# Optimization experiments

Hardware: AMD Instinct MI355X
Metric: run time of the kernel (lower is better)

## Reference

```python
import jax, jax.numpy as jnp
import numpy as np

NUM_USERS = 100000
NUM_ITEMS = 50000
N_NODES = NUM_USERS + NUM_ITEMS
EMBED_DIM = 64
NUM_LAYERS = 3
NUM_EDGES = 1250000
EDGE_ATTR_DIM = 7
MLP_HID = 32
AUDIO_SCALE = 1.0
META_SCALE = 0.5


def _l2norm(x, eps=1e-12):
    # F.normalize(p=2, dim=-1): x / max(||x||, eps)
    n = jnp.sqrt(jnp.sum(x * x, axis=-1, keepdims=True))
    return x / jnp.maximum(n, eps)


def setup_inputs() -> dict:
    key = jax.random.key(0)
    ks = jax.random.split(key, 12)
    return {
        'user_emb_w': jax.random.normal(ks[0], (NUM_USERS, EMBED_DIM), jnp.float32),
        'artist_emb_w': jax.random.normal(ks[1], (20000, EMBED_DIM), jnp.float32),
        'album_emb_w': jax.random.normal(ks[2], (40000, EMBED_DIM), jnp.float32),
        'item_audio': jax.random.normal(ks[3], (NUM_ITEMS, EMBED_DIM), jnp.float32),
        'edge_attr': jax.random.normal(ks[4], (NUM_EDGES, EDGE_ATTR_DIM), jnp.float32),
        'edge_weight_init': jax.random.uniform(ks[5], (NUM_EDGES,), jnp.float32),
        'w1': jax.random.normal(ks[6], (EDGE_ATTR_DIM + 1, MLP_HID), jnp.float32),
        'b1': jnp.zeros((MLP_HID,), jnp.float32),
        'w2': jax.random.normal(ks[7], (MLP_HID, 1), jnp.float32),
        'b2': jnp.zeros((1,), jnp.float32),
        'edge_index': jax.random.randint(ks[8], (2, NUM_EDGES), 0, N_NODES, jnp.int64 if jax.config.read('jax_enable_x64') else jnp.int32),
        'artist_ids': jax.random.randint(ks[9], (NUM_ITEMS,), 0, 20000, jnp.int32),
        'album_ids': jax.random.randint(ks[10], (NUM_ITEMS,), 0, 40000, jnp.int32),
    }


def reference(user_emb_w, artist_emb_w, album_emb_w, item_audio, edge_attr,
              edge_weight_init, w1, b1, w2, b2, edge_index, artist_ids, album_ids):
    # Edge weight MLP: Linear -> ReLU -> Linear -> Sigmoid, squeezed
    ef = jnp.concatenate([edge_attr, edge_weight_init[:, None]], axis=1)  # [E, 8]
    h = jax.nn.relu(ef @ w1 + b1)
    w = jax.nn.sigmoid(h @ w2 + b2)[:, 0]  # [E]

    # Node features
    user_embed = _l2norm(user_emb_w)                                   # [U, D]
    meta = (artist_emb_w[artist_ids] + album_emb_w[album_ids]) * META_SCALE
    item_embed = _l2norm(item_audio * AUDIO_SCALE + meta)              # [I, D]
    x = jnp.concatenate([user_embed, item_embed], axis=0)              # [N, D]

    # gcn_norm (LGConv default, no self-loops): deg from target (col) scatter of w
    row, col = edge_index[0], edge_index[1]
    deg = jax.ops.segment_sum(w, col, num_segments=N_NODES)
    dinv = jnp.where(deg > 0, jax.lax.rsqrt(jnp.maximum(deg, 1e-30)), 0.0)
    norm = dinv[row] * w * dinv[col]                                   # [E]

    acc = x
    for _ in range(NUM_LAYERS):
        msg = norm[:, None] * x[row]                                   # [E, D]
        x = jax.ops.segment_sum(msg, col, num_segments=N_NODES)       # [N, D]
        acc = acc + x
    x = _l2norm(acc / (NUM_LAYERS + 1))

    user_emb = x[:NUM_USERS]
    item_emb = x[NUM_USERS:]
    align_loss = jnp.float32(0.0)
    return user_emb, item_emb, align_loss
```

## Files before the change

### kernel.cpp

```cpp
#include <hip/hip_runtime.h>
#include <hip/hip_bf16.h>
#include <math.h>

#define NUM_USERS  100000
#define NUM_ITEMS  50000
#define N_NODES    150000
#define EMBED_DIM  64
#define NUM_EDGES  1250000
#define MLP_HID    32
#define SCAN_B     1024
#define SCAN_NB    ((N_NODES + SCAN_B - 1) / SCAN_B)

__global__ void hist_rank(const int* __restrict__ edge_index,
                          int* __restrict__ cnt,
                          int* __restrict__ rank) {
    int e = blockIdx.x * blockDim.x + threadIdx.x;
    if (e >= NUM_EDGES) return;
    int c = edge_index[NUM_EDGES + e];
    rank[e] = atomicAdd(&cnt[c], 1);
}

__global__ void scan_partial(const int* __restrict__ cnt,
                             int* __restrict__ part) {
    __shared__ int s[SCAN_B];
    int tid = threadIdx.x;
    int i = blockIdx.x * SCAN_B + tid;
    s[tid] = (i < N_NODES) ? cnt[i] : 0;
    __syncthreads();
#pragma unroll
    for (int off = SCAN_B / 2; off > 0; off >>= 1) {
        if (tid < off) s[tid] += s[tid + off];
        __syncthreads();
    }
    if (tid == 0) part[blockIdx.x] = s[0];
}

__global__ void scan_offsets(const int* __restrict__ part,
                             int* __restrict__ base_off) {
    __shared__ int s[256];
    int tid = threadIdx.x;
    int v = (tid < SCAN_NB) ? part[tid] : 0;
    s[tid] = v;
    __syncthreads();
#pragma unroll
    for (int off = 1; off < 256; off <<= 1) {
        int t = (tid >= off) ? s[tid - off] : 0;
        __syncthreads();
        s[tid] += t;
        __syncthreads();
    }
    if (tid < SCAN_NB) base_off[tid] = s[tid] - v;
}

__global__ void scan_apply(const int* __restrict__ cnt,
                           const int* __restrict__ base_off,
                           int* __restrict__ row_ptr) {
    __shared__ int s[SCAN_B];
    int tid = threadIdx.x;
    int i = blockIdx.x * SCAN_B + tid;
    int v = (i < N_NODES) ? cnt[i] : 0;
    s[tid] = v;
    __syncthreads();
    for (int off = 1; off < SCAN_B; off <<= 1) {
        int t = (tid >= off) ? s[tid - off] : 0;
        __syncthreads();
        s[tid] += t;
        __syncthreads();
    }
    if (i < N_NODES) row_ptr[i] = s[tid] - v + base_off[blockIdx.x];
    if (blockIdx.x == 0 && tid == 0) row_ptr[N_NODES] = NUM_EDGES;
}

__global__ void mlp_scatter(const float* __restrict__ edge_attr,
                            const float* __restrict__ ew,
                            const float* __restrict__ w1,
                            const float* __restrict__ b1,
                            const float* __restrict__ w2,
                            const float* __restrict__ b2,
                            const int*   __restrict__ edge_index,
                            const int*   __restrict__ rank,
                            const int*   __restrict__ row_ptr,
                            int2* __restrict__ csr_pair) {
    __shared__ float w1s[8 * MLP_HID];
    __shared__ float b1s[MLP_HID];
    __shared__ float w2s[MLP_HID];
    int tid = threadIdx.x;
    if (tid < 8 * MLP_HID) w1s[tid] = w1[tid];
    if (tid < MLP_HID) { b1s[tid] = b1[tid]; w2s[tid] = w2[tid]; }
    __syncthreads();

    int e = blockIdx.x * blockDim.x + tid;
    if (e >= NUM_EDGES) return;

    float ef[8];
#pragma unroll
    for (int k = 0; k < 7; ++k) ef[k] = edge_attr[e * 7 + k];
    ef[7] = ew[e];

    float s = b2[0];
#pragma unroll
    for (int j = 0; j < MLP_HID; ++j) {
        float h = b1s[j];
#pragma unroll
        for (int k = 0; k < 8; ++k) h = fmaf(ef[k], w1s[k * MLP_HID + j], h);
        h = fmaxf(h, 0.0f);
        s = fmaf(h, w2s[j], s);
    }
    float w = 1.0f / (1.0f + expf(-s));

    int r = edge_index[e];
    int c = edge_index[NUM_EDGES + e];
    int pos = row_ptr[c] + rank[e];
    int2 pr;
    pr.x = r;
    pr.y = __float_as_int(w);
    csr_pair[pos] = pr;
}

__global__ void deg_dinv_csr(const int* __restrict__ row_ptr,
                             const int2* __restrict__ csr_pair,
                             float* __restrict__ dinv) {
    int t = blockIdx.x * blockDim.x + threadIdx.x;
    int node = t >> 4;
    int lane = t & 15;
    if (node >= N_NODES) return;
    int s = row_ptr[node], e = row_ptr[node + 1];
    float sum = 0.0f;
    for (int j = s + lane; j < e; j += 16) sum += __int_as_float(csr_pair[j].y);
    sum += __shfl_xor(sum, 8);
    sum += __shfl_xor(sum, 4);
    sum += __shfl_xor(sum, 2);
    sum += __shfl_xor(sum, 1);
    if (lane == 0)
        dinv[node] = (sum > 0.0f) ? rsqrtf(fmaxf(sum, 1e-30f)) : 0.0f;
}

__global__ void csr_scale(const int* __restrict__ row_ptr,
                          const float* __restrict__ dinv,
                          int2* __restrict__ csr_pair) {
    int t = blockIdx.x * blockDim.x + threadIdx.x;
    int node = t >> 4;
    int lane = t & 15;
    if (node >= N_NODES) return;
    int s = row_ptr[node], e = row_ptr[node + 1];
    float dc = dinv[node];
    for (int j = s + lane; j < e; j += 16) {
        int2 p = csr_pair[j];
        p.y = __float_as_int(__int_as_float(p.y) * dc * dinv[p.x]);
        csr_pair[j] = p;
    }
}

__global__ void init_x(const float* __restrict__ user_w,
                       const float* __restrict__ artist_w,
                       const float* __restrict__ album_w,
                       const float* __restrict__ audio,
                       const int*   __restrict__ artist_ids,
                       const int*   __restrict__ album_ids,
                       __hip_bfloat16* __restrict__ x) {
    int t = blockIdx.x * blockDim.x + threadIdx.x;
    int row = t >> 6;
    int lane = t & 63;
    if (row >= N_NODES) return;

    float v;
    if (row < NUM_USERS) {
        v = user_w[row * EMBED_DIM + lane];
    } else {
        int r = row - NUM_USERS;
        int ar = artist_ids[r];
        int al = album_ids[r];
        v = audio[r * EMBED_DIM + lane]
          + 0.5f * (artist_w[ar * EMBED_DIM + lane] + album_w[al * EMBED_DIM + lane]);
    }
    float ss = v * v;
#pragma unroll
    for (int off = 32; off > 0; off >>= 1) ss += __shfl_xor(ss, off);
    float scale = 1.0f / fmaxf(sqrtf(ss), 1e-12f);
    x[row * EMBED_DIM + lane] = __float2bfloat16(v * scale);
}

__global__ void propagate_mid(const int* __restrict__ row_ptr,
                              const int2* __restrict__ csr_pair,
                              const unsigned short* __restrict__ xin,
                              unsigned short* __restrict__ xout) {
    int t = blockIdx.x * blockDim.x + threadIdx.x;
    int node = t >> 6;
    int lane = t & 63;
    if (node >= N_NODES) return;

    int start = row_ptr[node];
    int end   = row_ptr[node + 1];

    int eg = lane >> 4;
    int dq = (lane & 15) << 2;

    float a0 = 0, a1 = 0, a2 = 0, a3 = 0;

    int j = start + eg;
    int2 p = csr_pair[j];

    for (int base = start; base < end; base += 4) {
        bool ok = (base + eg < end);
        int   src = ok ? p.x : 0;
        float nw  = ok ? __int_as_float(p.y) : 0.0f;
        uint2 u = *(const uint2*)(xin + ((size_t)src << 6) + dq);
        j += 4;
        int2 pn = csr_pair[j];
        a0 = fmaf(nw, __uint_as_float(u.x << 16),         a0);
        a1 = fmaf(nw, __uint_as_float(u.x & 0xffff0000u), a1);
        a2 = fmaf(nw, __uint_as_float(u.y << 16),         a2);
        a3 = fmaf(nw, __uint_as_float(u.y & 0xffff0000u), a3);
        p = pn;
    }

    a0 += __shfl_xor(a0, 16); a1 += __shfl_xor(a1, 16);
    a2 += __shfl_xor(a2, 16); a3 += __shfl_xor(a3, 16);
    a0 += __shfl_xor(a0, 32); a1 += __shfl_xor(a1, 32);
    a2 += __shfl_xor(a2, 32); a3 += __shfl_xor(a3, 32);

    if (eg == 0) {
        size_t o = ((size_t)node << 6) + dq;
        unsigned int b0 = (unsigned int)__bfloat16_as_ushort(__float2bfloat16(a0));
        unsigned int b1 = (unsigned int)__bfloat16_as_ushort(__float2bfloat16(a1));
        unsigned int b2 = (unsigned int)__bfloat16_as_ushort(__float2bfloat16(a2));
        unsigned int b3 = (unsigned int)__bfloat16_as_ushort(__float2bfloat16(a3));
        uint2 u;
        u.x = b0 | (b1 << 16);
        u.y = b2 | (b3 << 16);
        *(uint2*)(xout + o) = u;
    }
}

__global__ void propagate_final(const int* __restrict__ row_ptr,
                                const int2* __restrict__ csr_pair,
                                const unsigned short* __restrict__ x0,
                                const unsigned short* __restrict__ x1,
                                const unsigned short* __restrict__ x2,
                                float* __restrict__ outp) {
    int t = blockIdx.x * blockDim.x + threadIdx.x;
    int node = t >> 6;
    int lane = t & 63;
    if (node >= N_NODES) return;

    int start = row_ptr[node];
    int end   = row_ptr[node + 1];

    int eg = lane >> 4;
    int dq = (lane & 15) << 2;

    float a0 = 0, a1 = 0, a2 = 0, a3 = 0;

    int j = start + eg;
    int2 p = csr_pair[j];

    for (int base = start; base < end; base += 4) {
        bool ok = (base + eg < end);
        int   src = ok ? p.x : 0;
        float nw  = ok ? __int_as_float(p.y) : 0.0f;
        uint2 u = *(const uint2*)(x2 + ((size_t)src << 6) + dq);
        j += 4;
        int2 pn = csr_pair[j];
        a0 = fmaf(nw, __uint_as_float(u.x << 16),         a0);
        a1 = fmaf(nw, __uint_as_float(u.x & 0xffff0000u), a1);
        a2 = fmaf(nw, __uint_as_float(u.y << 16),         a2);
        a3 = fmaf(nw, __uint_as_float(u.y & 0xffff0000u), a3);
        p = pn;
    }

    a0 += __shfl_xor(a0, 16); a1 += __shfl_xor(a1, 16);
    a2 += __shfl_xor(a2, 16); a3 += __shfl_xor(a3, 16);
    a0 += __shfl_xor(a0, 32); a1 += __shfl_xor(a1, 32);
    a2 += __shfl_xor(a2, 32); a3 += __shfl_xor(a3, 32);

    if (eg == 0) {
        size_t o = ((size_t)node << 6) + dq;
        uint2 u0 = *(const uint2*)(x0 + o);
        uint2 u1 = *(const uint2*)(x1 + o);
        uint2 u2 = *(const uint2*)(x2 + o);

#define BF_LO(u) __uint_as_float((u) << 16)
#define BF_HI(u) __uint_as_float((u) & 0xffff0000u)
        float v0 = (BF_LO(u0.x) + BF_LO(u1.x) + BF_LO(u2.x) + a0) * 0.25f;
        float v1 = (BF_HI(u0.x) + BF_HI(u1.x) + BF_HI(u2.x) + a1) * 0.25f;
        float v2 = (BF_LO(u0.y) + BF_LO(u1.y) + BF_LO(u2.y) + a2) * 0.25f;
        float v3 = (BF_HI(u0.y) + BF_HI(u1.y) + BF_HI(u2.y) + a3) * 0.25f;
#undef BF_LO
#undef BF_HI

        float ss = v0 * v0 + v1 * v1 + v2 * v2 + v3 * v3;
        ss += __shfl_xor(ss, 1);
        ss += __shfl_xor(ss, 2);
        ss += __shfl_xor(ss, 4);
        ss += __shfl_xor(ss, 8);
        float scale = 1.0f / fmaxf(sqrtf(ss), 1e-12f);

        float4 r = { v0 * scale, v1 * scale, v2 * scale, v3 * scale };
        *(float4*)(outp + o) = r;
    }
    if (blockIdx.x == 0 && threadIdx.x == 0)
        outp[(size_t)N_NODES * EMBED_DIM] = 0.0f;
}

extern "C" void kernel_launch(void* const* d_in, const int* in_sizes, int n_in,
                              void* d_out, int out_size, void* d_ws, size_t ws_size,
                              hipStream_t stream) {
    const float* user_w     = (const float*)d_in[0];
    const float* artist_w   = (const float*)d_in[1];
    const float* album_w    = (const float*)d_in[2];
    const float* audio      = (const float*)d_in[3];
    const float* edge_attr  = (const float*)d_in[4];
    const float* ew         = (const float*)d_in[5];
    const float* w1         = (const float*)d_in[6];
    const float* b1         = (const float*)d_in[7];
    const float* w2         = (const float*)d_in[8];
    const float* b2         = (const float*)d_in[9];
    const int*   edge_index = (const int*)d_in[10];
    const int*   artist_ids = (const int*)d_in[11];
    const int*   album_ids  = (const int*)d_in[12];
    float* out = (float*)d_out;

    float* ws = (float*)d_ws;
    unsigned short* x0 = (unsigned short*)ws;
    unsigned short* x1 = (unsigned short*)(ws + 4800000);
    unsigned short* x2 = (unsigned short*)(ws + 9600000);
    int*  row_ptr  = (int*)(ws + 14400000);
    int2* csr_pair = (int2*)(ws + 14560000);
    float* dinv    = ws + 17060000;
    int*   cnt     = (int*)ws;
    int*   rank    = (int*)(ws + 150000);
    int*   part    = (int*)(ws + 1400000);
    int*   baseoff = (int*)(ws + 1401000);

    const int B = 256;
    const int egrid = (NUM_EDGES + B - 1) / B;
    const int ngrid   = (N_NODES * EMBED_DIM) / B;
    const int ngrid16 = (N_NODES * 16) / B;

    hipMemsetAsync(cnt, 0, N_NODES * sizeof(int), stream);

    hist_rank<<<egrid, B, 0, stream>>>(edge_index, cnt, rank);

    scan_partial<<<SCAN_NB, SCAN_B, 0, stream>>>(cnt, part);
    scan_offsets<<<1, 256, 0, stream>>>(part, baseoff);
    scan_apply<<<SCAN_NB, SCAN_B, 0, stream>>>(cnt, baseoff, row_ptr);

    mlp_scatter<<<egrid, B, 0, stream>>>(
        edge_attr, ew, w1, b1, w2, b2, edge_index, rank, row_ptr, csr_pair);

    deg_dinv_csr<<<ngrid16, B, 0, stream>>>(row_ptr, csr_pair, dinv);
    csr_scale<<<ngrid16, B, 0, stream>>>(row_ptr, dinv, csr_pair);

    init_x<<<ngrid, B, 0, stream>>>(
        user_w, artist_w, album_w, audio, artist_ids, album_ids,
        (__hip_bfloat16*)x0);

    propagate_mid<<<ngrid, B, 0, stream>>>(row_ptr, csr_pair, x0, x1);
    propagate_mid<<<ngrid, B, 0, stream>>>(row_ptr, csr_pair, x1, x2);
    propagate_final<<<ngrid, B, 0, stream>>>(row_ptr, csr_pair, x0, x1, x2, out);
}
```

Measured before the change: 464.9 us.

## Process four nodes per wavefront with four-edge-per-lane gather in propagation

The propagation kernels now assign four consecutive destination nodes to each 64-lane wavefront instead of one. Each 16-lane group handles four edges per iteration, so sixteen edges are in flight per wave step. The row pointers are loaded once and broadcast with shuffles, and the next CSR pairs are prefetched. This targets low memory-level parallelism and wasted lanes on low-degree nodes (about 8 edges per node on average), but it serializes four nodes per wave, which can lengthen per-wave latency and hurt load balance.

Result: faster. 409.1 us (-12.0%).

```diff
diff --git a/kernel.cpp b/kernel.cpp
--- a/kernel.cpp
+++ b/kernel.cpp
@@ -10,6 +10,7 @@
 #define MLP_HID    32
 #define SCAN_B     1024
 #define SCAN_NB    ((N_NODES + SCAN_B - 1) / SCAN_B)
+#define NPW        4
 
 __global__ void hist_rank(const int* __restrict__ edge_index,
                           int* __restrict__ cnt,
@@ -180,55 +181,94 @@
     x[row * EMBED_DIM + lane] = __float2bfloat16(v * scale);
 }
 
+#define BF_LO(u) __uint_as_float((u) << 16)
+#define BF_HI(u) __uint_as_float((u) & 0xffff0000u)
+
 __global__ void propagate_mid(const int* __restrict__ row_ptr,
                               const int2* __restrict__ csr_pair,
                               const unsigned short* __restrict__ xin,
                               unsigned short* __restrict__ xout) {
-    int t = blockIdx.x * blockDim.x + threadIdx.x;
-    int node = t >> 6;
-    int lane = t & 63;
-    if (node >= N_NODES) return;
-
-    int start = row_ptr[node];
-    int end   = row_ptr[node + 1];
+    int wave = (blockIdx.x * blockDim.x + threadIdx.x) >> 6;
+    int lane = threadIdx.x & 63;
+    int node0 = wave * NPW;
+    if (node0 >= N_NODES) return;
 
     int eg = lane >> 4;
     int dq = (lane & 15) << 2;
 
-    float a0 = 0, a1 = 0, a2 = 0, a3 = 0;
-
-    int j = start + eg;
-    int2 p = csr_pair[j];
-
-    for (int base = start; base < end; base += 4) {
-        bool ok = (base + eg < end);
-        int   src = ok ? p.x : 0;
-        float nw  = ok ? __int_as_float(p.y) : 0.0f;
-        uint2 u = *(const uint2*)(xin + ((size_t)src << 6) + dq);
-        j += 4;
-        int2 pn = csr_pair[j];
-        a0 = fmaf(nw, __uint_as_float(u.x << 16),         a0);
-        a1 = fmaf(nw, __uint_as_float(u.x & 0xffff0000u), a1);
-        a2 = fmaf(nw, __uint_as_float(u.y << 16),         a2);
-        a3 = fmaf(nw, __uint_as_float(u.y & 0xffff0000u), a3);
-        p = pn;
-    }
-
-    a0 += __shfl_xor(a0, 16); a1 += __shfl_xor(a1, 16);
-    a2 += __shfl_xor(a2, 16); a3 += __shfl_xor(a3, 16);
-    a0 += __shfl_xor(a0, 32); a1 += __shfl_xor(a1, 32);
-    a2 += __shfl_xor(a2, 32); a3 += __shfl_xor(a3, 32);
-
-    if (eg == 0) {
-        size_t o = ((size_t)node << 6) + dq;
-        unsigned int b0 = (unsigned int)__bfloat16_as_ushort(__float2bfloat16(a0));
-        unsigned int b1 = (unsigned int)__bfloat16_as_ushort(__float2bfloat16(a1));
-        unsigned int b2 = (unsigned int)__bfloat16_as_ushort(__float2bfloat16(a2));
-        unsigned int b3 = (unsigned int)__bfloat16_as_ushort(__float2bfloat16(a3));
-        uint2 u;
-        u.x = b0 | (b1 << 16);
-        u.y = b2 | (b3 << 16);
-        *(uint2*)(xout + o) = u;
+    int rpv = row_ptr[node0 + (lane < NPW ? lane : NPW)];
+    int rs0 = __shfl(rpv, 0);
+    int rs1 = __shfl(rpv, 1);
+    int rs2 = __shfl(rpv, 2);
+    int rs3 = __shfl(rpv, 3);
+    int rs4 = __shfl(rpv, 4);
+    int rs[NPW + 1] = { rs0, rs1, rs2, rs3, rs4 };
+
+    int j = rs0 + (eg << 2);
+    int2 p0 = csr_pair[j];
+    int2 p1 = csr_pair[j + 1];
+    int2 p2 = csr_pair[j + 2];
+    int2 p3 = csr_pair[j + 3];
+
+#pragma unroll
+    for (int k = 0; k < NPW; ++k) {
+        int base = rs[k];
+        int e    = rs[k + 1];
+        float a0 = 0, a1 = 0, a2 = 0, a3 = 0;
+
+        while (true) {
+            int idx = base + (eg << 2);
+            bool o0 = idx     < e;
+            bool o1 = idx + 1 < e;
+            bool o2 = idx + 2 < e;
+            bool o3 = idx + 3 < e;
+            int   s0 = o0 ? p0.x : 0; float w0 = o0 ? __int_as_float(p0.y) : 0.0f;
+            int   s1 = o1 ? p1.x : 0; float w1 = o1 ? __int_as_float(p1.y) : 0.0f;
+            int   s2 = o2 ? p2.x : 0; float w2 = o2 ? __int_as_float(p2.y) : 0.0f;
+            int   s3 = o3 ? p3.x : 0; float w3 = o3 ? __int_as_float(p3.y) : 0.0f;
+
+            uint2 u0 = *(const uint2*)(xin + ((size_t)s0 << 6) + dq);
+            uint2 u1 = *(const uint2*)(xin + ((size_t)s1 << 6) + dq);
+            uint2 u2 = *(const uint2*)(xin + ((size_t)s2 << 6) + dq);
+            uint2 u3 = *(const uint2*)(xin + ((size_t)s3 << 6) + dq);
+
+            int  nbase = base + 16;
+            bool more  = nbase < e;
+            int  nj    = (more ? nbase : e) + (eg << 2);
+            p0 = csr_pair[nj];
+            p1 = csr_pair[nj + 1];
+            p2 = csr_pair[nj + 2];
+            p3 = csr_pair[nj + 3];
+
+            a0 = fmaf(w0, BF_LO(u0.x), a0); a1 = fmaf(w0, BF_HI(u0.x), a1);
+            a2 = fmaf(w0, BF_LO(u0.y), a2); a3 = fmaf(w0, BF_HI(u0.y), a3);
+            a0 = fmaf(w1, BF_LO(u1.x), a0); a1 = fmaf(w1, BF_HI(u1.x), a1);
+            a2 = fmaf(w1, BF_LO(u1.y), a2); a3 = fmaf(w1, BF_HI(u1.y), a3);
+            a0 = fmaf(w2, BF_LO(u2.x), a0); a1 = fmaf(w2, BF_HI(u2.x), a1);
+            a2 = fmaf(w2, BF_LO(u2.y), a2); a3 = fmaf(w2, BF_HI(u2.y), a3);
+            a0 = fmaf(w3, BF_LO(u3.x), a0); a1 = fmaf(w3, BF_HI(u3.x), a1);
+            a2 = fmaf(w3, BF_LO(u3.y), a2); a3 = fmaf(w3, BF_HI(u3.y), a3);
+
+            if (!more) break;
+            base = nbase;
+        }
+
+        a0 += __shfl_xor(a0, 16); a1 += __shfl_xor(a1, 16);
+        a2 += __shfl_xor(a2, 16); a3 += __shfl_xor(a3, 16);
+        a0 += __shfl_xor(a0, 32); a1 += __shfl_xor(a1, 32);
+        a2 += __shfl_xor(a2, 32); a3 += __shfl_xor(a3, 32);
+
+        if (eg == 0) {
+            size_t o = ((size_t)(node0 + k) << 6) + dq;
+            unsigned int b0 = (unsigned int)__bfloat16_as_ushort(__float2bfloat16(a0));
+            unsigned int b1 = (unsigned int)__bfloat16_as_ushort(__float2bfloat16(a1));
+            unsigned int b2 = (unsigned int)__bfloat16_as_ushort(__float2bfloat16(a2));
+            unsigned int b3 = (unsigned int)__bfloat16_as_ushort(__float2bfloat16(a3));
+            uint2 u;
+            u.x = b0 | (b1 << 16);
+            u.y = b2 | (b3 << 16);
+            *(uint2*)(xout + o) = u;
+        }
     }
 }
 
@@ -238,69 +278,104 @@
                                 const unsigned short* __restrict__ x1,
                                 const unsigned short* __restrict__ x2,
                                 float* __restrict__ outp) {
-    int t = blockIdx.x * blockDim.x + threadIdx.x;
-    int node = t >> 6;
-    int lane = t & 63;
-    if (node >= N_NODES) return;
-
-    int start = row_ptr[node];
-    int end   = row_ptr[node + 1];
+    int wave = (blockIdx.x * blockDim.x + threadIdx.x) >> 6;
+    int lane = threadIdx.x & 63;
+    int node0 = wave * NPW;
+    if (node0 >= N_NODES) return;
 
     int eg = lane >> 4;
     int dq = (lane & 15) << 2;
 
-    float a0 = 0, a1 = 0, a2 = 0, a3 = 0;
-
-    int j = start + eg;
-    int2 p = csr_pair[j];
-
-    for (int base = start; base < end; base += 4) {
-        bool ok = (base + eg < end);
-        int   src = ok ? p.x : 0;
-        float nw  = ok ? __int_as_float(p.y) : 0.0f;
-        uint2 u = *(const uint2*)(x2 + ((size_t)src << 6) + dq);
-        j += 4;
-        int2 pn = csr_pair[j];
-        a0 = fmaf(nw, __uint_as_float(u.x << 16),         a0);
-        a1 = fmaf(nw, __uint_as_float(u.x & 0xffff0000u), a1);
-        a2 = fmaf(nw, __uint_as_float(u.y << 16),         a2);
-        a3 = fmaf(nw, __uint_as_float(u.y & 0xffff0000u), a3);
-        p = pn;
-    }
-
-    a0 += __shfl_xor(a0, 16); a1 += __shfl_xor(a1, 16);
-    a2 += __shfl_xor(a2, 16); a3 += __shfl_xor(a3, 16);
-    a0 += __shfl_xor(a0, 32); a1 += __shfl_xor(a1, 32);
-    a2 += __shfl_xor(a2, 32); a3 += __shfl_xor(a3, 32);
-
-    if (eg == 0) {
-        size_t o = ((size_t)node << 6) + dq;
-        uint2 u0 = *(const uint2*)(x0 + o);
-        uint2 u1 = *(const uint2*)(x1 + o);
-        uint2 u2 = *(const uint2*)(x2 + o);
-
-#define BF_LO(u) __uint_as_float((u) << 16)
-#define BF_HI(u) __uint_as_float((u) & 0xffff0000u)
-        float v0 = (BF_LO(u0.x) + BF_LO(u1.x) + BF_LO(u2.x) + a0) * 0.25f;
-        float v1 = (BF_HI(u0.x) + BF_HI(u1.x) + BF_HI(u2.x) + a1) * 0.25f;
-        float v2 = (BF_LO(u0.y) + BF_LO(u1.y) + BF_LO(u2.y) + a2) * 0.25f;
-        float v3 = (BF_HI(u0.y) + BF_HI(u1.y) + BF_HI(u2.y) + a3) * 0.25f;
+    int rpv = row_ptr[node0 + (lane < NPW ? lane : NPW)];
+    int rs0 = __shfl(rpv, 0);
+    int rs1 = __shfl(rpv, 1);
+    int rs2 = __shfl(rpv, 2);
+    int rs3 = __shfl(rpv, 3);
+    int rs4 = __shfl(rpv, 4);
+    int rs[NPW + 1] = { rs0, rs1, rs2, rs3, rs4 };
+
+    int j = rs0 + (eg << 2);
+    int2 p0 = csr_pair[j];
+    int2 p1 = csr_pair[j + 1];
+    int2 p2 = csr_pair[j + 2];
+    int2 p3 = csr_pair[j + 3];
+
+#pragma unroll
+    for (int k = 0; k < NPW; ++k) {
+        int base = rs[k];
+        int e    = rs[k + 1];
+        float a0 = 0, a1 = 0, a2 = 0, a3 = 0;
+
+        while (true) {
+            int idx = base + (eg << 2);
+            bool o0 = idx     < e;
+            bool o1 = idx + 1 < e;
+            bool o2 = idx + 2 < e;
+            bool o3 = idx + 3 < e;
+            int   s0 = o0 ? p0.x : 0; float w0 = o0 ? __int_as_float(p0.y) : 0.0f;
+            int   s1 = o1 ? p1.x : 0; float w1 = o1 ? __int_as_float(p1.y) : 0.0f;
+            int   s2 = o2 ? p2.x : 0; float w2 = o2 ? __int_as_float(p2.y) : 0.0f;
+            int   s3 = o3 ? p3.x : 0; float w3 = o3 ? __int_as_float(p3.y) : 0.0f;
+
+            uint2 u0 = *(const uint2*)(x2 + ((size_t)s0 << 6) + dq);
+            uint2 u1 = *(const uint2*)(x2 + ((size_t)s1 << 6) + dq);
+            uint2 u2 = *(const uint2*)(x2 + ((size_t)s2 << 6) + dq);
+            uint2 u3 = *(const uint2*)(x2 + ((size_t)s3 << 6) + dq);
+
+            int  nbase = base + 16;
+            bool more  = nbase < e;
+            int  nj    = (more ? nbase : e) + (eg << 2);
+            p0 = csr_pair[nj];
+            p1 = csr_pair[nj + 1];
+            p2 = csr_pair[nj + 2];
+            p3 = csr_pair[nj + 3];
+
+            a0 = fmaf(w0, BF_LO(u0.x), a0); a1 = fmaf(w0, BF_HI(u0.x), a1);
+            a2 = fmaf(w0, BF_LO(u0.y), a2); a3 = fmaf(w0, BF_HI(u0.y), a3);
+            a0 = fmaf(w1, BF_LO(u1.x), a0); a1 = fmaf(w1, BF_HI(u1.x), a1);
+            a2 = fmaf(w1, BF_LO(u1.y), a2); a3 = fmaf(w1, BF_HI(u1.y), a3);
+            a0 = fmaf(w2, BF_LO(u2.x), a0); a1 = fmaf(w2, BF_HI(u2.x), a1);
+            a2 = fmaf(w2, BF_LO(u2.y), a2); a3 = fmaf(w2, BF_HI(u2.y), a3);
+            a0 = fmaf(w3, BF_LO(u3.x), a0); a1 = fmaf(w3, BF_HI(u3.x), a1);
+            a2 = fmaf(w3, BF_LO(u3.y), a2); a3 = fmaf(w3, BF_HI(u3.y), a3);
+
+            if (!more) break;
+            base = nbase;
+        }
+
+        a0 += __shfl_xor(a0, 16); a1 += __shfl_xor(a1, 16);
+        a2 += __shfl_xor(a2, 16); a3 += __shfl_xor(a3, 16);
+        a0 += __shfl_xor(a0, 32); a1 += __shfl_xor(a1, 32);
+        a2 += __shfl_xor(a2, 32); a3 += __shfl_xor(a3, 32);
+
+        if (eg == 0) {
+            size_t o = ((size_t)(node0 + k) << 6) + dq;
+            uint2 u0 = *(const uint2*)(x0 + o);
+            uint2 u1 = *(const uint2*)(x1 + o);
+            uint2 u2 = *(const uint2*)(x2 + o);
+
+            float v0 = (BF_LO(u0.x) + BF_LO(u1.x) + BF_LO(u2.x) + a0) * 0.25f;
+            float v1 = (BF_HI(u0.x) + BF_HI(u1.x) + BF_HI(u2.x) + a1) * 0.25f;
+            float v2 = (BF_LO(u0.y) + BF_LO(u1.y) + BF_LO(u2.y) + a2) * 0.25f;
+            float v3 = (BF_HI(u0.y) + BF_HI(u1.y) + BF_HI(u2.y) + a3) * 0.25f;
+
+            float ss = v0 * v0 + v1 * v1 + v2 * v2 + v3 * v3;
+            ss += __shfl_xor(ss, 1);
+            ss += __shfl_xor(ss, 2);
+            ss += __shfl_xor(ss, 4);
+            ss += __shfl_xor(ss, 8);
+            float scale = 1.0f / fmaxf(sqrtf(ss), 1e-12f);
+
+            float4 r = { v0 * scale, v1 * scale, v2 * scale, v3 * scale };
+            *(float4*)(outp + o) = r;
+        }
+    }
+    if (blockIdx.x == 0 && threadIdx.x == 0)
+        outp[(size_t)N_NODES * EMBED_DIM] = 0.0f;
+}
+
 #undef BF_LO
 #undef BF_HI
-
-        float ss = v0 * v0 + v1 * v1 + v2 * v2 + v3 * v3;
-        ss += __shfl_xor(ss, 1);
-        ss += __shfl_xor(ss, 2);
-        ss += __shfl_xor(ss, 4);
-        ss += __shfl_xor(ss, 8);
-        float scale = 1.0f / fmaxf(sqrtf(ss), 1e-12f);
-
-        float4 r = { v0 * scale, v1 * scale, v2 * scale, v3 * scale };
-        *(float4*)(outp + o) = r;
-    }
-    if (blockIdx.x == 0 && threadIdx.x == 0)
-        outp[(size_t)N_NODES * EMBED_DIM] = 0.0f;
-}
 
 extern "C" void kernel_launch(void* const* d_in, const int* in_sizes, int n_in,
                               void* d_out, int out_size, void* d_ws, size_t ws_size,
@@ -336,6 +411,7 @@
     const int egrid = (NUM_EDGES + B - 1) / B;
     const int ngrid   = (N_NODES * EMBED_DIM) / B;
     const int ngrid16 = (N_NODES * 16) / B;
+    const int pgrid   = (N_NODES / NPW * 64) / B;
 
     hipMemsetAsync(cnt, 0, N_NODES * sizeof(int), stream);
 
@@ -355,7 +431,7 @@
         user_w, artist_w, album_w, audio, artist_ids, album_ids,
         (__hip_bfloat16*)x0);
 
-    propagate_mid<<<ngrid, B, 0, stream>>>(row_ptr, csr_pair, x0, x1);
-    propagate_mid<<<ngrid, B, 0, stream>>>(row_ptr, csr_pair, x1, x2);
-    propagate_final<<<ngrid, B, 0, stream>>>(row_ptr, csr_pair, x0, x1, x2, out);
-}
+    propagate_mid<<<pgrid, B, 0, stream>>>(row_ptr, csr_pair, x0, x1);
+    propagate_mid<<<pgrid, B, 0, stream>>>(row_ptr, csr_pair, x1, x2);
+    propagate_final<<<pgrid, B, 0, stream>>>(row_ptr, csr_pair, x0, x1, x2, out);
+}
```
